# Kernel optimization log

Measured on AMD Instinct MI355X. Metric: run time of the kernel, lower is better.

The kernel has to match this reference:

```python
import jax, jax.numpy as jnp
import numpy as np

N, E = 10000, 160000
HID, EDIM = 256, 128
EPS = 1e-5


def _layernorm(x, g, b):
    mu = jnp.mean(x, axis=-1, keepdims=True)
    var = jnp.mean(jnp.square(x - mu), axis=-1, keepdims=True)
    return (x - mu) * jax.lax.rsqrt(var + EPS) * g + b


def setup_inputs() -> dict:
    key = jax.random.key(0)
    ks = jax.random.split(key, 12)
    cat_dim = 2 * HID + EDIM  # 640

    def lin(k, fan_in, fan_out):
        kw, kb = jax.random.split(k)
        lim = 1.0 / np.sqrt(fan_in)
        W = jax.random.uniform(kw, (fan_in, fan_out), jnp.float32, -lim, lim)
        b = jax.random.uniform(kb, (fan_out,), jnp.float32, -lim, lim)
        return W, b

    We1, be1 = lin(ks[0], cat_dim, EDIM)
    We2, be2 = lin(ks[1], EDIM, EDIM)
    Wv1, bv1 = lin(ks[2], cat_dim, HID)
    Wv2, bv2 = lin(ks[3], HID, HID)

    return {
        "h": jax.random.normal(ks[4], (N, HID), jnp.float32),
        "e": jax.random.normal(ks[5], (E, EDIM), jnp.float32),
        "edge_index": jax.random.randint(ks[6], (2, E), 0, N, jnp.int64),
        "We1": We1, "be1": be1, "We2": We2, "be2": be2,
        "Wv1": Wv1, "bv1": bv1, "Wv2": Wv2, "bv2": bv2,
        "ne_g": jnp.ones((EDIM,), jnp.float32), "ne_b": jnp.zeros((EDIM,), jnp.float32),
        "nv_g": jnp.ones((HID,), jnp.float32), "nv_b": jnp.zeros((HID,), jnp.float32),
    }


def reference(h, e, edge_index, We1, be1, We2, be2, Wv1, bv1, Wv2, bv2,
              ne_g, ne_b, nv_g, nv_b):
    # Eval mode: dropout and edge_drop are identity.
    src, dst = edge_index[0], edge_index[1]
    h_src = h[src]  # [E, HID] gather
    h_dst = h[dst]  # [E, HID] gather

    # Edge update: phi_e(concat) -> residual + LayerNorm
    xe = jnp.concatenate([h_src, h_dst, e], axis=-1)  # [E, 2H+ED]
    e_msg = jax.nn.gelu(xe @ We1 + be1, approximate=False) @ We2 + be2
    e_new = _layernorm(e + e_msg, ne_g, ne_b)

    # Node update: phi_v(concat with updated e) -> scatter_mean -> residual + LN
    xv = jnp.concatenate([h_src, h_dst, e_new], axis=-1)
    m = jax.nn.gelu(xv @ Wv1 + bv1, approximate=False) @ Wv2 + bv2  # [E, HID]
    agg = jax.ops.segment_sum(m, dst, num_segments=h.shape[0])
    counts = jax.ops.segment_sum(jnp.ones((m.shape[0], 1), m.dtype), dst,
                                 num_segments=h.shape[0])
    agg = agg / jnp.maximum(counts, 1.0)
    h_new = _layernorm(h + agg, nv_g, nv_b)
    return (h_new, e_new)
```

## Files before the change

### kernel.cpp

```cpp
#include <hip/hip_runtime.h>
#include <hip/hip_bf16.h>

#define NNODE 10000
#define NEDGE 160000
#define HIDD  256
#define ED    128
#define CAT   640

typedef short bf8 __attribute__((ext_vector_type(8)));
typedef short bf4 __attribute__((ext_vector_type(4)));
typedef float f4  __attribute__((ext_vector_type(4)));
typedef unsigned int u32;

__device__ __forceinline__ float bf2f(ushort u) {
    return __uint_as_float(((unsigned)u) << 16);
}
__device__ __forceinline__ ushort f2bf(float f) {
    unsigned u = __float_as_uint(f);
    return (ushort)((u + 0x7fffu + ((u >> 16) & 1u)) >> 16);
}
__device__ __forceinline__ float gelu_exact(float x) {
    return 0.5f * x * (1.0f + erff(x * 0.70710678118654752f));
}
__device__ __forceinline__ int clampi(int v) {
    return ((unsigned)v >= (unsigned)NNODE) ? 0 : v;
}
__device__ __forceinline__ int getidx(const int* ei, bool i64, int pos) {
    int v = i64 ? ei[2 * pos] : ei[pos];
    return clampi(v);
}
__device__ __forceinline__ float loadf(const void* p, size_t idx, bool f32) {
    return f32 ? ((const float*)p)[idx] : bf2f(((const ushort*)p)[idx]);
}
__device__ __forceinline__ bf8 load8(const void* p, size_t idx, bool f32) {
    if (f32) {
        const float* fp = (const float*)p + idx;
        f4 lo = *(const f4*)fp, hi = *(const f4*)(fp + 4);
        bf8 r;
        r[0] = (short)f2bf(lo[0]); r[1] = (short)f2bf(lo[1]);
        r[2] = (short)f2bf(lo[2]); r[3] = (short)f2bf(lo[3]);
        r[4] = (short)f2bf(hi[0]); r[5] = (short)f2bf(hi[1]);
        r[6] = (short)f2bf(hi[2]); r[7] = (short)f2bf(hi[3]);
        return r;
    }
    return *(const bf8*)((const ushort*)p + idx);
}
__device__ __forceinline__ void storef(void* p, size_t idx, float v, bool f32) {
    if (f32) ((float*)p)[idx] = v;
    else     ((ushort*)p)[idx] = f2bf(v);
}
__device__ __forceinline__ void fadd_native(float* p, float v) {
    unsafeAtomicAdd(p, v);
}

__global__ void detect_kernel(const u32* __restrict__ h_u32,
                              const u32* __restrict__ ei_u32,
                              u32* __restrict__ flags) {
    int t = threadIdx.x;
    u32 e8 = (h_u32[t] >> 7) & 0xFFu;
    bool inw = (e8 >= 100u && e8 <= 150u);
    unsigned long long m = __ballot(inw);
    bool hi_nz = (t < 16) ? (ei_u32[2 * t + 1] != 0u) : false;
    unsigned long long m2 = __ballot(hi_nz);
    if (t == 0) {
        flags[0] = (__popcll(m) < 40) ? 1u : 0u;
        flags[1] = (m2 == 0ull) ? 1u : 0u;
    }
}

__global__ void prep_kernel(const void* __restrict__ We1, const void* __restrict__ We2,
                            const void* __restrict__ Wv1, const void* __restrict__ Wv2,
                            ushort* __restrict__ WT, const u32* __restrict__ flags) {
    const bool f32 = flags[0] != 0;
    int idx = blockIdx.x * 256 + threadIdx.x;
    if (idx >= 327680) return;
    const void* W; int base, k0, K, Wld;
    if      (idx <  32768) { W = We1; base = 0;      k0 = 0;   K = 256; Wld = 128; }
    else if (idx <  65536) { W = We1; base = 32768;  k0 = 256; K = 256; Wld = 128; }
    else if (idx <  81920) { W = We1; base = 65536;  k0 = 512; K = 128; Wld = 128; }
    else if (idx <  98304) { W = We2; base = 81920;  k0 = 0;   K = 128; Wld = 128; }
    else if (idx < 163840) { W = Wv1; base = 98304;  k0 = 0;   K = 256; Wld = 256; }
    else if (idx < 229376) { W = Wv1; base = 163840; k0 = 256; K = 256; Wld = 256; }
    else if (idx < 262144) { W = Wv1; base = 229376; k0 = 512; K = 128; Wld = 256; }
    else                   { W = Wv2; base = 262144; k0 = 0;   K = 256; Wld = 256; }
    int local = idx - base;
    int k = local & (K - 1);
    int n = local / K;
    WT[idx] = f2bf(loadf(W, (size_t)(k0 + k) * Wld + n, f32));
}

__global__ void hconv_kernel(const void* __restrict__ h, ushort* __restrict__ hb,
                             const u32* __restrict__ flags) {
    const bool f32 = flags[0] != 0;
    int i = blockIdx.x * 256 + threadIdx.x;
    if (i < NNODE * HIDD / 8)
        *(bf8*)&hb[(size_t)i * 8] = load8(h, (size_t)i * 8, f32);
}

__global__ void count_kernel(const int* __restrict__ ei, u32* __restrict__ cnt,
                             const u32* __restrict__ flags) {
    bool i64 = flags[1] != 0;
    int i = blockIdx.x * 256 + threadIdx.x;
    if (i < NEDGE) atomicAdd(&cnt[getidx(ei, i64, NEDGE + i)], 1u);
}

__global__ void scan_kernel(const u32* __restrict__ cnt, int* __restrict__ head) {
    __shared__ u32 part[256];
    __shared__ u32 base[256];
    int t = threadIdx.x;
    u32 s = 0;
    for (int j = 0; j < 40; ++j) {
        int i = t * 40 + j;
        if (i < NNODE) s += cnt[i];
    }
    part[t] = s;
    __syncthreads();
    if (t == 0) {
        u32 run = 0;
        for (int i = 0; i < 256; ++i) { base[i] = run; run += part[i]; }
    }
    __syncthreads();
    u32 run = base[t];
    for (int j = 0; j < 40; ++j) {
        int i = t * 40 + j;
        if (i < NNODE) { head[i] = (int)run; run += cnt[i]; }
    }
}

__global__ void fill_kernel(const int* __restrict__ ei, int* __restrict__ head,
                            int* __restrict__ perm, int* __restrict__ dsts,
                            const u32* __restrict__ flags) {
    bool i64 = flags[1] != 0;
    int i = blockIdx.x * 256 + threadIdx.x;
    if (i < NEDGE) {
        int d = getidx(ei, i64, NEDGE + i);
        int pos = atomicAdd(&head[d], 1);
        perm[pos] = i;
        dsts[pos] = d;
    }
}

template<int NB>
__device__ __forceinline__ void qp_body(const ushort* __restrict__ hb,
                                        const ushort* __restrict__ WT,
                                        const void* __restrict__ bias,
                                        ushort* __restrict__ O, int bid, bool f32) {
    const int tid = threadIdx.x;
    const int wid = tid >> 6, lane = tid & 63;
    const int l16 = lane & 15, lg = lane >> 4;
    const int node0 = bid * 64;
    const int N = NB * 64;
    const int n0 = wid * (NB * 16);

    size_t ra[4];
    #pragma unroll
    for (int ai = 0; ai < 4; ++ai) {
        int row = node0 + ai * 16 + l16;
        ra[ai] = (size_t)(row < NNODE ? row : NNODE - 1) * HIDD;
    }
    int bb[NB];
    #pragma unroll
    for (int bi = 0; bi < NB; ++bi) bb[bi] = (n0 + bi * 16 + l16) * HIDD;

    f4 acc[4][NB] = {};
    for (int kc = 0; kc < 4; ++kc) {
        #pragma unroll
        for (int ks = 0; ks < 2; ++ks) {
            int kk = kc * 64 + ks * 32 + lg * 8;
            bf8 b[NB];
            #pragma unroll
            for (int bi = 0; bi < NB; ++bi) b[bi] = *(const bf8*)&WT[bb[bi] + kk];
            #pragma unroll
            for (int ai = 0; ai < 4; ++ai) {
                bf8 a = *(const bf8*)&hb[ra[ai] + kk];
                #pragma unroll
                for (int bi = 0; bi < NB; ++bi)
                    acc[ai][bi] = __builtin_amdgcn_mfma_f32_16x16x32_bf16(a, b[bi], acc[ai][bi], 0, 0, 0);
            }
        }
    }
    #pragma unroll
    for (int bi = 0; bi < NB; ++bi) {
        int col = n0 + bi * 16 + l16;
        int pcol; float badd;
        if constexpr (NB == 4) {
            int hh = col >> 7, c = col & 127;
            badd = (hh == 0) ? loadf(bias, c, f32) : 0.f;
            pcol = hh * 128 + (c & 15) * 8 + (c >> 4);
        } else {
            int hh = col >> 8, c = col & 255;
            badd = (hh == 0) ? loadf(bias, c, f32) : 0.f;
            int nh2 = c >> 7, rem = c & 127, w = rem >> 5, b2 = (rem >> 4) & 1, l = c & 15;
            pcol = hh * 256 + w * 64 + l * 4 + nh2 * 2 + b2;
        }
        #pragma unroll
        for (int ai = 0; ai < 4; ++ai)
            #pragma unroll
            for (int r = 0; r < 4; ++r) {
                int gr = node0 + ai * 16 + lg * 4 + r;
                if (gr < NNODE) O[(size_t)gr * N + pcol] = f2bf(acc[ai][bi][r] + badd);
            }
    }
}

#define QPB ((NNODE + 63) / 64)
__global__ __launch_bounds__(256) void qp2_kernel(
    const ushort* __restrict__ hb, const ushort* __restrict__ WTe,
    const ushort* __restrict__ WTv, const void* __restrict__ be1,
    const void* __restrict__ bv1, ushort* __restrict__ Qab,
    ushort* __restrict__ Pab, const u32* __restrict__ flags) {
    const bool f32 = flags[0] != 0;
    if (blockIdx.x < QPB) qp_body<4>(hb, WTe, be1, Qab, blockIdx.x, f32);
    else                  qp_body<8>(hb, WTv, bv1, Pab, blockIdx.x - QPB, f32);
}

__global__ __launch_bounds__(256) void fused_kernel(
    const void* __restrict__ e, const int* __restrict__ ei,
    const int* __restrict__ perm, const int* __restrict__ dsts,
    const ushort* __restrict__ WT1c,
    const ushort* __restrict__ WT2, const void* __restrict__ be2,
    const ushort* __restrict__ Qab,
    const void* __restrict__ neg, const void* __restrict__ neb,
    const ushort* __restrict__ WvcT,
    const ushort* __restrict__ Pab,
    float* __restrict__ S, void* __restrict__ out,
    const u32* __restrict__ flags)
{
    const bool f32 = flags[0] != 0, i64 = flags[1] != 0;
    __shared__ ushort Asm[64 * 72];
    __shared__ ushort Bsm[128 * 72];
    __shared__ ushort Tsm[64 * 136];
    __shared__ int PermS[64], SrcS[64], DstS[64];

    const int tid = threadIdx.x;
    const int wid = tid >> 6, lane = tid & 63;
    const int l16 = lane & 15, lg = lane >> 4;
    const int edge0 = blockIdx.x * 64;
    const int rm = wid * 16;

    if (tid < 64) {
        int eid = perm[edge0 + tid];
        PermS[tid] = eid;
        SrcS[tid] = getidx(ei, i64, eid);
        DstS[tid] = dsts[edge0 + tid];
    }
    __syncthreads();

    f4 acc[8] = {};
    for (int kc = 0; kc < 2; ++kc) {
        __syncthreads();
        #pragma unroll
        for (int half = 0; half < 2; ++half) {
            int slot = tid + half * 256;
            int r = slot >> 3, c8 = (slot & 7) * 8;
            int eid = PermS[r];
            *(bf8*)&Asm[r * 72 + c8] = load8(e, (size_t)eid * ED + kc * 64 + c8, f32);
        }
        #pragma unroll
        for (int it = 0; it < 4; ++it) {
            int slot = tid + it * 256;
            int n = slot >> 3, c8 = (slot & 7) * 8;
            *(bf8*)&Bsm[n * 72 + c8] = *(const bf8*)&WT1c[n * 128 + kc * 64 + c8];
        }
        __syncthreads();
        #pragma unroll
        for (int ks = 0; ks < 2; ++ks) {
            bf8 a = *(const bf8*)&Asm[(rm + l16) * 72 + ks * 32 + lg * 8];
            #pragma unroll
            for (int f = 0; f < 8; ++f) {
                bf8 b = *(const bf8*)&Bsm[(f * 16 + l16) * 72 + ks * 32 + lg * 8];
                acc[f] = __builtin_amdgcn_mfma_f32_16x16x32_bf16(a, b, acc[f], 0, 0, 0);
            }
        }
    }

    int sidx[4], didx[4];
    #pragma unroll
    for (int r = 0; r < 4; ++r) {
        int row = rm + lg * 4 + r;
        sidx[r] = SrcS[row];
        didx[r] = DstS[row];
    }
    bf8 qs[4], qd[4];
    #pragma unroll
    for (int r = 0; r < 4; ++r) {
        qs[r] = *(const bf8*)&Qab[(size_t)sidx[r] * 256 + l16 * 8];
        qd[r] = *(const bf8*)&Qab[(size_t)didx[r] * 256 + 128 + l16 * 8];
    }
    #pragma unroll
    for (int f = 0; f < 8; ++f) {
        #pragma unroll
        for (int r = 0; r < 4; ++r) {
            float val = acc[f][r] + bf2f((ushort)qs[r][f]) + bf2f((ushort)qd[r][f]);
            Tsm[(rm + lg * 4 + r) * 136 + f * 16 + l16] = f2bf(gelu_exact(val));
        }
    }

    f4 acc2[8] = {};
    for (int kc = 0; kc < 2; ++kc) {
        __syncthreads();
        #pragma unroll
        for (int it = 0; it < 4; ++it) {
            int slot = tid + it * 256;
            int n = slot >> 3, c8 = (slot & 7) * 8;
            *(bf8*)&Bsm[n * 72 + c8] = *(const bf8*)&WT2[n * 128 + kc * 64 + c8];
        }
        __syncthreads();
        #pragma unroll
        for (int ks = 0; ks < 2; ++ks) {
            bf8 a = *(const bf8*)&Tsm[(rm + l16) * 136 + kc * 64 + ks * 32 + lg * 8];
            #pragma unroll
            for (int f = 0; f < 8; ++f) {
                bf8 b = *(const bf8*)&Bsm[(f * 16 + l16) * 72 + ks * 32 + lg * 8];
                acc2[f] = __builtin_amdgcn_mfma_f32_16x16x32_bf16(a, b, acc2[f], 0, 0, 0);
            }
        }
    }

    float v[8][4];
    #pragma unroll
    for (int f = 0; f < 8; ++f) {
        int col = f * 16 + l16;
        float bias = loadf(be2, col, f32);
        #pragma unroll
        for (int r = 0; r < 4; ++r) {
            int row = rm + lg * 4 + r;
            v[f][r] = acc2[f][r] + bias
                    + loadf(e, (size_t)PermS[row] * ED + col, f32);
        }
    }
    #pragma unroll
    for (int r = 0; r < 4; ++r) {
        float s = 0.f;
        #pragma unroll
        for (int f = 0; f < 8; ++f) s += v[f][r];
        s += __shfl_xor(s, 1); s += __shfl_xor(s, 2);
        s += __shfl_xor(s, 4); s += __shfl_xor(s, 8);
        float mu = s * (1.0f / 128.0f);
        float q = 0.f;
        #pragma unroll
        for (int f = 0; f < 8; ++f) { float d = v[f][r] - mu; q += d * d; }
        q += __shfl_xor(q, 1); q += __shfl_xor(q, 2);
        q += __shfl_xor(q, 4); q += __shfl_xor(q, 8);
        float rstd = rsqrtf(q * (1.0f / 128.0f) + 1e-5f);
        int row = rm + lg * 4 + r;
        int eid = PermS[row];
        #pragma unroll
        for (int f = 0; f < 8; ++f) {
            int col = f * 16 + l16;
            float y = (v[f][r] - mu) * rstd * loadf(neg, col, f32) + loadf(neb, col, f32);
            storef(out, (size_t)NNODE * HIDD + (size_t)eid * ED + col, y, f32);
            Tsm[row * 136 + col] = f2bf(y);
        }
    }

    f4 accN[4][2][2] = {};
    #pragma unroll
    for (int nh = 0; nh < 2; ++nh) {
        for (int kc = 0; kc < 2; ++kc) {
            __syncthreads();
            #pragma unroll
            for (int it = 0; it < 4; ++it) {
                int slot = tid + it * 256;
                int n = slot >> 3, c8 = (slot & 7) * 8;
                *(bf8*)&Bsm[n * 72 + c8] = *(const bf8*)&WvcT[(nh * 128 + n) * 128 + kc * 64 + c8];
            }
            __syncthreads();
            #pragma unroll
            for (int ks = 0; ks < 2; ++ks) {
                bf8 a[4], b[2];
                #pragma unroll
                for (int ai = 0; ai < 4; ++ai)
                    a[ai] = *(const bf8*)&Tsm[(ai * 16 + l16) * 136 + kc * 64 + ks * 32 + lg * 8];
                #pragma unroll
                for (int bi = 0; bi < 2; ++bi)
                    b[bi] = *(const bf8*)&Bsm[(wid * 32 + bi * 16 + l16) * 72 + ks * 32 + lg * 8];
                #pragma unroll
                for (int ai = 0; ai < 4; ++ai)
                    #pragma unroll
                    for (int bi = 0; bi < 2; ++bi)
                        accN[ai][nh][bi] = __builtin_amdgcn_mfma_f32_16x16x32_bf16(a[ai], b[bi], accN[ai][nh][bi], 0, 0, 0);
            }
        }
    }

    #pragma unroll
    for (int ai = 0; ai < 4; ++ai) {
        int p0 = ai * 16 + lg * 4;
        int dd[4], ss[4];
        #pragma unroll
        for (int r = 0; r < 4; ++r) { dd[r] = DstS[p0 + r]; ss[r] = SrcS[p0 + r]; }
        bf4 ps[4], pd[4];
        #pragma unroll
        for (int r = 0; r < 4; ++r) {
            ps[r] = *(const bf4*)&Pab[(size_t)ss[r] * 512 + wid * 64 + l16 * 4];
            pd[r] = *(const bf4*)&Pab[(size_t)dd[r] * 512 + 256 + wid * 64 + l16 * 4];
        }
        #pragma unroll
        for (int nh = 0; nh < 2; ++nh)
            #pragma unroll
            for (int bi = 0; bi < 2; ++bi) {
                int col = nh * 128 + wid * 32 + bi * 16 + l16;
                const int j = nh * 2 + bi;
                float v0 = gelu_exact(accN[ai][nh][bi][0] + bf2f((ushort)ps[0][j]) + bf2f((ushort)pd[0][j]));
                float v1 = gelu_exact(accN[ai][nh][bi][1] + bf2f((ushort)ps[1][j]) + bf2f((ushort)pd[1][j]));
                float v2 = gelu_exact(accN[ai][nh][bi][2] + bf2f((ushort)ps[2][j]) + bf2f((ushort)pd[2][j]));
                float v3 = gelu_exact(accN[ai][nh][bi][3] + bf2f((ushort)ps[3][j]) + bf2f((ushort)pd[3][j]));
                float s = v0; int d = dd[0];
                if (dd[1] == d) s += v1; else { fadd_native(&S[(size_t)d * HIDD + col], s); d = dd[1]; s = v1; }
                if (dd[2] == d) s += v2; else { fadd_native(&S[(size_t)d * HIDD + col], s); d = dd[2]; s = v2; }
                if (dd[3] == d) s += v3; else { fadd_native(&S[(size_t)d * HIDD + col], s); d = dd[3]; s = v3; }
                fadd_native(&S[(size_t)d * HIDD + col], s);
            }
    }
}

__global__ __launch_bounds__(256) void hn_gemm_kernel(
    const float* __restrict__ S, const ushort* __restrict__ WTv2,
    const void* __restrict__ bv2, const u32* __restrict__ cnt,
    const void* __restrict__ h,
    const void* __restrict__ nvg, const void* __restrict__ nvb,
    void* __restrict__ out, const u32* __restrict__ flags)
{
    const bool f32 = flags[0] != 0;
    constexpr int LDV = 260;
    __shared__ float Vsm[64 * LDV];

    const int tid = threadIdx.x;
    const int wid = tid >> 6, lane = tid & 63;
    const int l16 = lane & 15, lg = lane >> 4;
    const int node0 = blockIdx.x * 64;
    const int n0 = wid * 64;

    size_t ra[4];
    #pragma unroll
    for (int ai = 0; ai < 4; ++ai) {
        int row = node0 + ai * 16 + l16;
        ra[ai] = (size_t)(row < NNODE ? row : NNODE - 1) * HIDD;
    }
    int bb[4];
    #pragma unroll
    for (int bi = 0; bi < 4; ++bi) bb[bi] = (n0 + bi * 16 + l16) * HIDD;

    f4 acc[4][4] = {};
    for (int kc = 0; kc < 4; ++kc) {
        #pragma unroll
        for (int ks = 0; ks < 2; ++ks) {
            int kk = kc * 64 + ks * 32 + lg * 8;
            bf8 b[4];
            #pragma unroll
            for (int bi = 0; bi < 4; ++bi) b[bi] = *(const bf8*)&WTv2[bb[bi] + kk];
            #pragma unroll
            for (int ai = 0; ai < 4; ++ai) {
                bf8 a = load8(S, ra[ai] + kk, true);
                #pragma unroll
                for (int bi = 0; bi < 4; ++bi)
                    acc[ai][bi] = __builtin_amdgcn_mfma_f32_16x16x32_bf16(a, b[bi], acc[ai][bi], 0, 0, 0);
            }
        }
    }

    #pragma unroll
    for (int bi = 0; bi < 4; ++bi) {
        int col = n0 + bi * 16 + l16;
        float b2 = loadf(bv2, col, f32);
        #pragma unroll
        for (int ai = 0; ai < 4; ++ai)
            #pragma unroll
            for (int r = 0; r < 4; ++r) {
                int rowl = ai * 16 + lg * 4 + r;
                int gr = node0 + rowl;
                int grc = gr < NNODE ? gr : NNODE - 1;
                float c = (float)cnt[grc];
                float inv = 1.0f / fmaxf(c, 1.0f);
                float val = (acc[ai][bi][r] + c * b2) * inv
                          + loadf(h, (size_t)grc * HIDD + col, f32);
                Vsm[rowl * LDV + col] = val;
            }
    }
    __syncthreads();

    #pragma unroll
    for (int rr = 0; rr < 4; ++rr) {
        int rowl = wid * 16 + lg * 4 + rr;
        int gr = node0 + rowl;
        float x[16];
        #pragma unroll
        for (int f = 0; f < 16; ++f) x[f] = Vsm[rowl * LDV + f * 16 + l16];
        float s = 0.f;
        #pragma unroll
        for (int f = 0; f < 16; ++f) s += x[f];
        s += __shfl_xor(s, 1); s += __shfl_xor(s, 2);
        s += __shfl_xor(s, 4); s += __shfl_xor(s, 8);
        float mu = s * (1.0f / 256.0f);
        float q = 0.f;
        #pragma unroll
        for (int f = 0; f < 16; ++f) { float d = x[f] - mu; q += d * d; }
        q += __shfl_xor(q, 1); q += __shfl_xor(q, 2);
        q += __shfl_xor(q, 4); q += __shfl_xor(q, 8);
        float rstd = rsqrtf(q * (1.0f / 256.0f) + 1e-5f);
        if (gr < NNODE) {
            #pragma unroll
            for (int f = 0; f < 16; ++f) {
                int col = f * 16 + l16;
                float y = (x[f] - mu) * rstd * loadf(nvg, col, f32) + loadf(nvb, col, f32);
                storef(out, (size_t)gr * HIDD + col, y, f32);
            }
        }
    }
}

extern "C" void kernel_launch(void* const* d_in, const int* in_sizes, int n_in,
                              void* d_out, int out_size, void* d_ws, size_t ws_size,
                              hipStream_t stream)
{
    (void)in_sizes; (void)n_in; (void)out_size; (void)ws_size;
    const void* h   = d_in[0];
    const void* e   = d_in[1];
    const int*  ei  = (const int*)d_in[2];
    const void* We1 = d_in[3];
    const void* be1 = d_in[4];
    const void* We2 = d_in[5];
    const void* be2 = d_in[6];
    const void* Wv1 = d_in[7];
    const void* bv1 = d_in[8];
    const void* Wv2 = d_in[9];
    const void* bv2 = d_in[10];
    const void* neg = d_in[11];
    const void* neb = d_in[12];
    const void* nvg = d_in[13];
    const void* nvb = d_in[14];

    char* ws = (char*)d_ws;
    u32*   flags = (u32*)ws;
    float* S     = (float*)(ws + 256);
    u32*   cnt   = (u32*)(ws + 256 + (size_t)NNODE * HIDD * 4);
    size_t off = 256 + (size_t)NNODE * HIDD * 4 + ((size_t)NNODE * 4 + 255) / 256 * 256;
    int*   head = (int*)(ws + off);            off += ((size_t)NNODE * 4 + 255) / 256 * 256;
    int*   perm = (int*)(ws + off);            off += (size_t)NEDGE * 4;
    int*   dsts = (int*)(ws + off);            off += (size_t)NEDGE * 4;
    ushort* WTb  = (ushort*)(ws + off);
    ushort* WTe  = WTb;
    ushort* WT1c = WTb + 65536;
    ushort* WT2  = WTb + 81920;
    ushort* WTv  = WTb + 98304;
    ushort* WvcT = WTb + 229376;
    ushort* WTv2 = WTb + 262144;
    ushort* hb   = WTb + 327680;
    ushort* Qab  = hb + (size_t)NNODE * HIDD;
    ushort* Pab  = Qab + (size_t)NNODE * 256;

    hipMemsetAsync(S, 0, (size_t)NNODE * HIDD * 4 + (size_t)NNODE * 4, stream);
    detect_kernel<<<1, 64, 0, stream>>>((const u32*)h, (const u32*)ei, flags);

    prep_kernel<<<1280, 256, 0, stream>>>(We1, We2, Wv1, Wv2, WTb, flags);
    hconv_kernel<<<(NNODE * HIDD / 8 + 255) / 256, 256, 0, stream>>>(h, hb, flags);
    count_kernel<<<(NEDGE + 255) / 256, 256, 0, stream>>>(ei, cnt, flags);
    scan_kernel<<<1, 256, 0, stream>>>(cnt, head);
    fill_kernel<<<(NEDGE + 255) / 256, 256, 0, stream>>>(ei, head, perm, dsts, flags);

    qp2_kernel<<<2 * QPB, 256, 0, stream>>>(hb, WTe, WTv, be1, bv1, Qab, Pab, flags);

    fused_kernel<<<NEDGE / 64, 256, 0, stream>>>(e, ei, perm, dsts,
                                                 WT1c, WT2, be2, Qab,
                                                 neg, neb, WvcT, Pab,
                                                 S, d_out, flags);
    hn_gemm_kernel<<<(NNODE + 63) / 64, 256, 0, stream>>>(S, WTv2, bv2, cnt, h,
                                                          nvg, nvb, d_out, flags);
}
```

Baseline: 369.9 us.

## Double fused kernel tile to 128 edges, remap blocks per XCD, use tanh GELU

```diff
diff --git a/kernel.cpp b/kernel.cpp
--- a/kernel.cpp
+++ b/kernel.cpp
@@ -19,8 +19,14 @@
     unsigned u = __float_as_uint(f);
     return (ushort)((u + 0x7fffu + ((u >> 16) & 1u)) >> 16);
 }
-__device__ __forceinline__ float gelu_exact(float x) {
-    return 0.5f * x * (1.0f + erff(x * 0.70710678118654752f));
+__device__ __forceinline__ float gelu_fast(float x) {
+    float x2 = x * x;
+    float u = 0.7978845608028654f * x * (1.0f + 0.044715f * x2);
+    float au = fabsf(u);
+    float ex = __expf(2.0f * au);
+    float t = 1.0f - 2.0f / (1.0f + ex);
+    t = copysignf(t, u);
+    return 0.5f * x * (1.0f + t);
 }
 __device__ __forceinline__ int clampi(int v) {
     return ((unsigned)v >= (unsigned)NNODE) ? 0 : v;
@@ -214,7 +220,8 @@
     else                  qp_body<8>(hb, WTv, bv1, Pab, blockIdx.x - QPB, f32);
 }
 
-__global__ __launch_bounds__(256) void fused_kernel(
+#define FWG (NEDGE / 128)
+__global__ __launch_bounds__(512) void fused_kernel(
     const void* __restrict__ e, const int* __restrict__ ei,
     const int* __restrict__ perm, const int* __restrict__ dsts,
     const ushort* __restrict__ WT1c,
@@ -227,18 +234,22 @@
     const u32* __restrict__ flags)
 {
     const bool f32 = flags[0] != 0, i64 = flags[1] != 0;
-    __shared__ ushort Asm[64 * 72];
+    __shared__ ushort Asm[128 * 72];
     __shared__ ushort Bsm[128 * 72];
-    __shared__ ushort Tsm[64 * 136];
-    __shared__ int PermS[64], SrcS[64], DstS[64];
+    __shared__ ushort Tsm[128 * 136];
+    __shared__ int PermS[128], SrcS[128], DstS[128];
+
+    int orig = blockIdx.x;
+    int xcd = orig & 7, slot = orig >> 3;
+    int bid = (xcd < 2 ? xcd * 157 : 2 * 157 + (xcd - 2) * 156) + slot;
 
     const int tid = threadIdx.x;
     const int wid = tid >> 6, lane = tid & 63;
     const int l16 = lane & 15, lg = lane >> 4;
-    const int edge0 = blockIdx.x * 64;
+    const int edge0 = bid * 128;
     const int rm = wid * 16;
 
-    if (tid < 64) {
+    if (tid < 128) {
         int eid = perm[edge0 + tid];
         PermS[tid] = eid;
         SrcS[tid] = getidx(ei, i64, eid);
@@ -251,15 +262,15 @@
         __syncthreads();
         #pragma unroll
         for (int half = 0; half < 2; ++half) {
-            int slot = tid + half * 256;
-            int r = slot >> 3, c8 = (slot & 7) * 8;
+            int slot2 = tid + half * 512;
+            int r = slot2 >> 3, c8 = (slot2 & 7) * 8;
             int eid = PermS[r];
             *(bf8*)&Asm[r * 72 + c8] = load8(e, (size_t)eid * ED + kc * 64 + c8, f32);
         }
         #pragma unroll
-        for (int it = 0; it < 4; ++it) {
-            int slot = tid + it * 256;
-            int n = slot >> 3, c8 = (slot & 7) * 8;
+        for (int it = 0; it < 2; ++it) {
+            int slot2 = tid + it * 512;
+            int n = slot2 >> 3, c8 = (slot2 & 7) * 8;
             *(bf8*)&Bsm[n * 72 + c8] = *(const bf8*)&WT1c[n * 128 + kc * 64 + c8];
         }
         __syncthreads();
@@ -274,25 +285,27 @@
         }
     }
 
-    int sidx[4], didx[4];
-    #pragma unroll
-    for (int r = 0; r < 4; ++r) {
-        int row = rm + lg * 4 + r;
-        sidx[r] = SrcS[row];
-        didx[r] = DstS[row];
-    }
-    bf8 qs[4], qd[4];
-    #pragma unroll
-    for (int r = 0; r < 4; ++r) {
-        qs[r] = *(const bf8*)&Qab[(size_t)sidx[r] * 256 + l16 * 8];
-        qd[r] = *(const bf8*)&Qab[(size_t)didx[r] * 256 + 128 + l16 * 8];
-    }
-    #pragma unroll
-    for (int f = 0; f < 8; ++f) {
+    {
+        int sidx[4], didx[4];
         #pragma unroll
         for (int r = 0; r < 4; ++r) {
-            float val = acc[f][r] + bf2f((ushort)qs[r][f]) + bf2f((ushort)qd[r][f]);
-            Tsm[(rm + lg * 4 + r) * 136 + f * 16 + l16] = f2bf(gelu_exact(val));
+            int row = rm + lg * 4 + r;
+            sidx[r] = SrcS[row];
+            didx[r] = DstS[row];
+        }
+        bf8 qs[4], qd[4];
+        #pragma unroll
+        for (int r = 0; r < 4; ++r) {
+            qs[r] = *(const bf8*)&Qab[(size_t)sidx[r] * 256 + l16 * 8];
+            qd[r] = *(const bf8*)&Qab[(size_t)didx[r] * 256 + 128 + l16 * 8];
+        }
+        #pragma unroll
+        for (int f = 0; f < 8; ++f) {
+            #pragma unroll
+            for (int r = 0; r < 4; ++r) {
+                float val = acc[f][r] + bf2f((ushort)qs[r][f]) + bf2f((ushort)qd[r][f]);
+                Tsm[(rm + lg * 4 + r) * 136 + f * 16 + l16] = f2bf(gelu_fast(val));
+            }
         }
     }
 
@@ -300,9 +313,9 @@
     for (int kc = 0; kc < 2; ++kc) {
         __syncthreads();
         #pragma unroll
-        for (int it = 0; it < 4; ++it) {
-            int slot = tid + it * 256;
-            int n = slot >> 3, c8 = (slot & 7) * 8;
+        for (int it = 0; it < 2; ++it) {
+            int slot2 = tid + it * 512;
+            int n = slot2 >> 3, c8 = (slot2 & 7) * 8;
             *(bf8*)&Bsm[n * 72 + c8] = *(const bf8*)&WT2[n * 128 + kc * 64 + c8];
         }
         __syncthreads();
@@ -317,52 +330,55 @@
         }
     }
 
-    float v[8][4];
-    #pragma unroll
-    for (int f = 0; f < 8; ++f) {
-        int col = f * 16 + l16;
-        float bias = loadf(be2, col, f32);
-        #pragma unroll
-        for (int r = 0; r < 4; ++r) {
-            int row = rm + lg * 4 + r;
-            v[f][r] = acc2[f][r] + bias
-                    + loadf(e, (size_t)PermS[row] * ED + col, f32);
-        }
-    }
-    #pragma unroll
-    for (int r = 0; r < 4; ++r) {
-        float s = 0.f;
-        #pragma unroll
-        for (int f = 0; f < 8; ++f) s += v[f][r];
-        s += __shfl_xor(s, 1); s += __shfl_xor(s, 2);
-        s += __shfl_xor(s, 4); s += __shfl_xor(s, 8);
-        float mu = s * (1.0f / 128.0f);
-        float q = 0.f;
-        #pragma unroll
-        for (int f = 0; f < 8; ++f) { float d = v[f][r] - mu; q += d * d; }
-        q += __shfl_xor(q, 1); q += __shfl_xor(q, 2);
-        q += __shfl_xor(q, 4); q += __shfl_xor(q, 8);
-        float rstd = rsqrtf(q * (1.0f / 128.0f) + 1e-5f);
-        int row = rm + lg * 4 + r;
-        int eid = PermS[row];
+    {
+        float v[8][4];
         #pragma unroll
         for (int f = 0; f < 8; ++f) {
             int col = f * 16 + l16;
-            float y = (v[f][r] - mu) * rstd * loadf(neg, col, f32) + loadf(neb, col, f32);
-            storef(out, (size_t)NNODE * HIDD + (size_t)eid * ED + col, y, f32);
-            Tsm[row * 136 + col] = f2bf(y);
-        }
-    }
-
+            float bias = loadf(be2, col, f32);
+            #pragma unroll
+            for (int r = 0; r < 4; ++r) {
+                int row = rm + lg * 4 + r;
+                v[f][r] = acc2[f][r] + bias
+                        + loadf(e, (size_t)PermS[row] * ED + col, f32);
+            }
+        }
+        #pragma unroll
+        for (int r = 0; r < 4; ++r) {
+            float s = 0.f;
+            #pragma unroll
+            for (int f = 0; f < 8; ++f) s += v[f][r];
+            s += __shfl_xor(s, 1); s += __shfl_xor(s, 2);
+            s += __shfl_xor(s, 4); s += __shfl_xor(s, 8);
+            float mu = s * (1.0f / 128.0f);
+            float q = 0.f;
+            #pragma unroll
+            for (int f = 0; f < 8; ++f) { float d = v[f][r] - mu; q += d * d; }
+            q += __shfl_xor(q, 1); q += __shfl_xor(q, 2);
+            q += __shfl_xor(q, 4); q += __shfl_xor(q, 8);
+            float rstd = rsqrtf(q * (1.0f / 128.0f) + 1e-5f);
+            int row = rm + lg * 4 + r;
+            int eid = PermS[row];
+            #pragma unroll
+            for (int f = 0; f < 8; ++f) {
+                int col = f * 16 + l16;
+                float y = (v[f][r] - mu) * rstd * loadf(neg, col, f32) + loadf(neb, col, f32);
+                storef(out, (size_t)NNODE * HIDD + (size_t)eid * ED + col, y, f32);
+                Tsm[row * 136 + col] = f2bf(y);
+            }
+        }
+    }
+
+    const int wr = wid >> 2, wc = wid & 3;
     f4 accN[4][2][2] = {};
     #pragma unroll
     for (int nh = 0; nh < 2; ++nh) {
         for (int kc = 0; kc < 2; ++kc) {
             __syncthreads();
             #pragma unroll
-            for (int it = 0; it < 4; ++it) {
-                int slot = tid + it * 256;
-                int n = slot >> 3, c8 = (slot & 7) * 8;
+            for (int it = 0; it < 2; ++it) {
+                int slot2 = tid + it * 512;
+                int n = slot2 >> 3, c8 = (slot2 & 7) * 8;
                 *(bf8*)&Bsm[n * 72 + c8] = *(const bf8*)&WvcT[(nh * 128 + n) * 128 + kc * 64 + c8];
             }
             __syncthreads();
@@ -371,10 +387,10 @@
                 bf8 a[4], b[2];
                 #pragma unroll
                 for (int ai = 0; ai < 4; ++ai)
-                    a[ai] = *(const bf8*)&Tsm[(ai * 16 + l16) * 136 + kc * 64 + ks * 32 + lg * 8];
+                    a[ai] = *(const bf8*)&Tsm[(wr * 64 + ai * 16 + l16) * 136 + kc * 64 + ks * 32 + lg * 8];
                 #pragma unroll
                 for (int bi = 0; bi < 2; ++bi)
-                    b[bi] = *(const bf8*)&Bsm[(wid * 32 + bi * 16 + l16) * 72 + ks * 32 + lg * 8];
+                    b[bi] = *(const bf8*)&Bsm[(wc * 32 + bi * 16 + l16) * 72 + ks * 32 + lg * 8];
                 #pragma unroll
                 for (int ai = 0; ai < 4; ++ai)
                     #pragma unroll
@@ -386,26 +402,26 @@
 
     #pragma unroll
     for (int ai = 0; ai < 4; ++ai) {
-        int p0 = ai * 16 + lg * 4;
+        int p0 = wr * 64 + ai * 16 + lg * 4;
         int dd[4], ss[4];
         #pragma unroll
         for (int r = 0; r < 4; ++r) { dd[r] = DstS[p0 + r]; ss[r] = SrcS[p0 + r]; }
         bf4 ps[4], pd[4];
         #pragma unroll
         for (int r = 0; r < 4; ++r) {
-            ps[r] = *(const bf4*)&Pab[(size_t)ss[r] * 512 + wid * 64 + l16 * 4];
-            pd[r] = *(const bf4*)&Pab[(size_t)dd[r] * 512 + 256 + wid * 64 + l16 * 4];
+            ps[r] = *(const bf4*)&Pab[(size_t)ss[r] * 512 + wc * 64 + l16 * 4];
+            pd[r] = *(const bf4*)&Pab[(size_t)dd[r] * 512 + 256 + wc * 64 + l16 * 4];
         }
         #pragma unroll
         for (int nh = 0; nh < 2; ++nh)
             #pragma unroll
             for (int bi = 0; bi < 2; ++bi) {
-                int col = nh * 128 + wid * 32 + bi * 16 + l16;
+                int col = nh * 128 + wc * 32 + bi * 16 + l16;
                 const int j = nh * 2 + bi;
-                float v0 = gelu_exact(accN[ai][nh][bi][0] + bf2f((ushort)ps[0][j]) + bf2f((ushort)pd[0][j]));
-                float v1 = gelu_exact(accN[ai][nh][bi][1] + bf2f((ushort)ps[1][j]) + bf2f((ushort)pd[1][j]));
-                float v2 = gelu_exact(accN[ai][nh][bi][2] + bf2f((ushort)ps[2][j]) + bf2f((ushort)pd[2][j]));
-                float v3 = gelu_exact(accN[ai][nh][bi][3] + bf2f((ushort)ps[3][j]) + bf2f((ushort)pd[3][j]));
+                float v0 = gelu_fast(accN[ai][nh][bi][0] + bf2f((ushort)ps[0][j]) + bf2f((ushort)pd[0][j]));
+                float v1 = gelu_fast(accN[ai][nh][bi][1] + bf2f((ushort)ps[1][j]) + bf2f((ushort)pd[1][j]));
+                float v2 = gelu_fast(accN[ai][nh][bi][2] + bf2f((ushort)ps[2][j]) + bf2f((ushort)pd[2][j]));
+                float v3 = gelu_fast(accN[ai][nh][bi][3] + bf2f((ushort)ps[3][j]) + bf2f((ushort)pd[3][j]));
                 float s = v0; int d = dd[0];
                 if (dd[1] == d) s += v1; else { fadd_native(&S[(size_t)d * HIDD + col], s); d = dd[1]; s = v1; }
                 if (dd[2] == d) s += v2; else { fadd_native(&S[(size_t)d * HIDD + col], s); d = dd[2]; s = v2; }
@@ -561,10 +577,10 @@
 
     qp2_kernel<<<2 * QPB, 256, 0, stream>>>(hb, WTe, WTv, be1, bv1, Qab, Pab, flags);
 
-    fused_kernel<<<NEDGE / 64, 256, 0, stream>>>(e, ei, perm, dsts,
-                                                 WT1c, WT2, be2, Qab,
-                                                 neg, neb, WvcT, Pab,
-                                                 S, d_out, flags);
+    fused_kernel<<<FWG, 512, 0, stream>>>(e, ei, perm, dsts,
+                                          WT1c, WT2, be2, Qab,
+                                          neg, neb, WvcT, Pab,
+                                          S, d_out, flags);
     hn_gemm_kernel<<<(NNODE + 63) / 64, 256, 0, stream>>>(S, WTv2, bv2, cnt, h,
                                                           nvg, nvb, d_out, flags);
 }
```

After: 361.7 us. -2.2%, faster.
